# Kernel optimization log

Measured on AMD Instinct MI355X. Metric: run time of the kernel, lower is better.

Reference implementation:

```python
import jax, jax.numpy as jnp
import numpy as np
import math

H = 8
D_MODEL = 512
D_K = D_MODEL // H          # 64, per-head value dim
D_QK = D_K // 2             # 32, per-head query/key dim
B, S = 2, 4096


def setup_inputs() -> dict:
    key = jax.random.key(0)
    ks = jax.random.split(key, 20)
    std = 0.02
    inp = {
        'query': jax.random.normal(ks[0], (B, S, D_MODEL), jnp.float32),
        'key':   jax.random.normal(ks[1], (B, S, D_MODEL), jnp.float32),
        'value': jax.random.normal(ks[2], (B, S, D_MODEL), jnp.float32),
        # MLP_q: d_model -> 2*d_model -> d_model/2
        'Wq1': jax.random.normal(ks[3], (D_MODEL, 2 * D_MODEL), jnp.float32) * std,
        'bq1': jnp.zeros((2 * D_MODEL,), jnp.float32),
        'Wq2': jax.random.normal(ks[4], (2 * D_MODEL, D_MODEL // 2), jnp.float32) * std,
        'bq2': jnp.zeros((D_MODEL // 2,), jnp.float32),
        # MLP_k: d_model -> 2*d_model -> d_model/2
        'Wk1': jax.random.normal(ks[5], (D_MODEL, 2 * D_MODEL), jnp.float32) * std,
        'bk1': jnp.zeros((2 * D_MODEL,), jnp.float32),
        'Wk2': jax.random.normal(ks[6], (2 * D_MODEL, D_MODEL // 2), jnp.float32) * std,
        'bk2': jnp.zeros((D_MODEL // 2,), jnp.float32),
        # linear_v and output linear: d_model -> d_model
        'Wv': jax.random.normal(ks[7], (D_MODEL, D_MODEL), jnp.float32) * std,
        'bv': jnp.zeros((D_MODEL,), jnp.float32),
        'Wo': jax.random.normal(ks[8], (D_MODEL, D_MODEL), jnp.float32) * std,
        'bo': jnp.zeros((D_MODEL,), jnp.float32),
    }
    return inp


def reference(query, key, value, Wq1, bq1, Wq2, bq2, Wk1, bk1, Wk2, bk2, Wv, bv, Wo, bo):
    nb = query.shape[0]
    # MLP_q / MLP_k: Linear -> exact GELU -> Linear (torch GELU default is erf)
    q = jax.nn.gelu(query @ Wq1 + bq1, approximate=False) @ Wq2 + bq2   # [B,S,D_MODEL/2]
    k = jax.nn.gelu(key   @ Wk1 + bk1, approximate=False) @ Wk2 + bk2   # [B,S,D_MODEL/2]
    v = value @ Wv + bv                                                  # [B,S,D_MODEL]

    q = q.reshape(nb, -1, H, D_QK)   # [B,S,H,d_qk]
    k = k.reshape(nb, -1, H, D_QK)
    v = v.reshape(nb, -1, H, D_K)    # [B,S,H,d_k]

    # scores scaled by sqrt(d_qk) since query.size(-1) == d_k//2 in the original
    scores = jnp.einsum('bqhd,bkhd->bhqk', q, k) / math.sqrt(D_QK)  # [B,H,S,S]
    p = jax.nn.softmax(scores, axis=-1)
    x = jnp.einsum('bhqk,bkhd->bqhd', p, v).reshape(nb, -1, H * D_K)  # [B,S,D_MODEL]
    return x @ Wo + bo
```

## Files before the change

kernel.cpp:

```cpp
#include <hip/hip_runtime.h>
#include <math.h>

typedef __attribute__((ext_vector_type(8))) short short8;
typedef __bf16 bf16x8 __attribute__((ext_vector_type(8)));
typedef __attribute__((ext_vector_type(4))) float f32x4;
typedef __attribute__((ext_vector_type(2))) float f32x2;
typedef __attribute__((ext_vector_type(16))) float f32x16;
typedef __attribute__((ext_vector_type(4))) unsigned uint4v;

__device__ inline short f2bf(float f) {
    unsigned u = __builtin_bit_cast(unsigned, f);
    u += 0x7fff + ((u >> 16) & 1);
    return (short)(u >> 16);
}
__device__ inline float gelu_f(float x) {
    return 0.5f * x * (1.f + erff(x * 0.70710678118654752f));
}

__device__ inline void gload_lds16(const void* g, void* l) {
    __builtin_amdgcn_global_load_lds(
        (const __attribute__((address_space(1))) unsigned int*)g,
        (__attribute__((address_space(3))) unsigned int*)l, 16, 0, 0);
}

__global__ __launch_bounds__(256) void prep_w(
    const float* __restrict__ Wq1, const float* __restrict__ Wk1,
    const float* __restrict__ Wq2, const float* __restrict__ Wk2,
    const float* __restrict__ Wv,  const float* __restrict__ Wo,
    short* __restrict__ Wq1t, short* __restrict__ Wk1t,
    short* __restrict__ Wq2t, short* __restrict__ Wk2t,
    short* __restrict__ Wvt,  short* __restrict__ Wot)
{
    int id = blockIdx.x;
    const float* W; short* Wt; int K, N;
    if (id < 512)       { W = Wq1; Wt = Wq1t; K = 512;  N = 1024; }
    else if (id < 1024) { W = Wk1; Wt = Wk1t; K = 512;  N = 1024; id -= 512; }
    else if (id < 1280) { W = Wq2; Wt = Wq2t; K = 1024; N = 256;  id -= 1024; }
    else if (id < 1536) { W = Wk2; Wt = Wk2t; K = 1024; N = 256;  id -= 1280; }
    else if (id < 1792) { W = Wv;  Wt = Wvt;  K = 512;  N = 512;  id -= 1536; }
    else                { W = Wo;  Wt = Wot;  K = 512;  N = 512;  id -= 1792; }
    int nx = N >> 5;
    int n0 = (id % nx) * 32, k0 = (id / nx) * 32;

    __shared__ float T[32][33];
    int tid = threadIdx.x;
    int r = tid >> 3, c4 = (tid & 7) * 4;
    float4 v4 = *(const float4*)&W[(size_t)(k0 + r) * N + n0 + c4];
    T[r][c4 + 0] = v4.x; T[r][c4 + 1] = v4.y; T[r][c4 + 2] = v4.z; T[r][c4 + 3] = v4.w;
    __syncthreads();
    short4 o;
    o.x = f2bf(T[c4 + 0][r]);
    o.y = f2bf(T[c4 + 1][r]);
    o.z = f2bf(T[c4 + 2][r]);
    o.w = f2bf(T[c4 + 3][r]);
    *(short4*)&Wt[(size_t)(n0 + r) * K + k0 + c4] = o;
}

template <int BM, int BN, int AF32>
__device__ __forceinline__ void gemm_core(
    const void* __restrict__ A, const short* __restrict__ B,
    const float* __restrict__ bias, void* __restrict__ C_,
    float scale, int act, int om, int nbn, int N, int K, int L)
{
    constexpr int MT = BM / 32;
    constexpr int NT = BN / 32;
    const int xcd = L & 7;
    const int per = L >> 3;
    const int bn = (per % nbn) * BN;
    const int bm = ((per / nbn) * 8 + xcd) * BM;

    const int tid = threadIdx.x;
    const int w = tid >> 6;
    const int lane = tid & 63;
    const int l15 = lane & 15, quad = lane >> 4;
    const int wm = (w >> 1) * (BM / 2), wn = (w & 1) * (BN / 2);

    __shared__ __align__(16) short As[2][BM * 64];
    __shared__ __align__(16) short Bs[2][BN * 64];

    const float* Af = (const float*)A;
    const short* Ab = (const short*)A;

    float4 xa[BM / 32], ya[BM / 32];

    auto stage_issue = [&](int k0, int buf) {
#pragma unroll
        for (int i = 0; i < BM / 32; ++i) {
            int ga = tid + i * 256;
            int row = ga >> 3, g = ga & 7;
            if constexpr (AF32) {
                const float* src = &Af[(size_t)(bm + row) * K + k0 + ((g ^ (row & 7)) * 8)];
                xa[i] = *(const float4*)src;
                ya[i] = *(const float4*)(src + 4);
            } else {
                gload_lds16(&Ab[(size_t)(bm + row) * K + k0 + ((g ^ (row & 7)) * 8)],
                            &As[buf][(i * 256 + w * 64) * 8]);
            }
        }
#pragma unroll
        for (int i = 0; i < BN / 32; ++i) {
            int gb = tid + i * 256;
            int row = gb >> 3, g = gb & 7;
            gload_lds16(&B[(size_t)(bn + row) * K + k0 + ((g ^ (row & 7)) * 8)],
                        &Bs[buf][(i * 256 + w * 64) * 8]);
        }
    };
    auto stage_finish = [&](int buf) {
        asm volatile("s_waitcnt vmcnt(0)");
        if constexpr (AF32) {
#pragma unroll
            for (int i = 0; i < BM / 32; ++i) {
                int ga = tid + i * 256;
                int row = ga >> 3, g = ga & 7;
                unsigned u0, u1, u2, u3;
                asm("v_cvt_pk_bf16_f32 %0, %1, %2" : "=v"(u0) : "v"(xa[i].x), "v"(xa[i].y));
                asm("v_cvt_pk_bf16_f32 %0, %1, %2" : "=v"(u1) : "v"(xa[i].z), "v"(xa[i].w));
                asm("v_cvt_pk_bf16_f32 %0, %1, %2" : "=v"(u2) : "v"(ya[i].x), "v"(ya[i].y));
                asm("v_cvt_pk_bf16_f32 %0, %1, %2" : "=v"(u3) : "v"(ya[i].z), "v"(ya[i].w));
                uint4v u; u[0] = u0; u[1] = u1; u[2] = u2; u[3] = u3;
                *(uint4v*)(void*)&As[buf][row * 64 + g * 8] = u;
            }
        }
    };

    f32x4 acc[MT][NT];
#pragma unroll
    for (int mt = 0; mt < MT; ++mt)
#pragma unroll
        for (int nt = 0; nt < NT; ++nt) acc[mt][nt] = (f32x4){0.f, 0.f, 0.f, 0.f};

    const int ntile = K >> 6;

    stage_issue(0, 0);
    stage_finish(0);
    __syncthreads();

    int cur = 0;
    for (int t = 0; t < ntile; ++t) {
        const bool has_next = (t + 1 < ntile);
        if (has_next) stage_issue((t + 1) << 6, cur ^ 1);

        const short* Asc = As[cur];
        const short* Bsc = Bs[cur];
#pragma unroll
        for (int ks = 0; ks < 2; ++ks) {
            bf16x8 af[MT], bfr[NT];
#pragma unroll
            for (int t2 = 0; t2 < MT; ++t2) {
                int row = wm + t2 * 16 + l15;
                af[t2] = __builtin_bit_cast(bf16x8,
                    *(const short8*)(const void*)&Asc[row * 64 + (((ks * 4 + quad) ^ (row & 7)) * 8)]);
            }
#pragma unroll
            for (int t2 = 0; t2 < NT; ++t2) {
                int row = wn + t2 * 16 + l15;
                bfr[t2] = __builtin_bit_cast(bf16x8,
                    *(const short8*)(const void*)&Bsc[row * 64 + (((ks * 4 + quad) ^ (row & 7)) * 8)]);
            }
#pragma unroll
            for (int mt = 0; mt < MT; ++mt)
#pragma unroll
                for (int nt = 0; nt < NT; ++nt)
                    acc[mt][nt] = __builtin_amdgcn_mfma_f32_16x16x32_bf16(af[mt], bfr[nt], acc[mt][nt], 0, 0, 0);
        }

        if (has_next) stage_finish(cur ^ 1);
        __syncthreads();
        cur ^= 1;
    }

    float bvv[NT];
#pragma unroll
    for (int nt = 0; nt < NT; ++nt) bvv[nt] = bias[bn + wn + nt * 16 + l15];
#pragma unroll
    for (int mt = 0; mt < MT; ++mt)
#pragma unroll
        for (int r = 0; r < 4; ++r) {
            int row = bm + wm + mt * 16 + quad * 4 + r;
#pragma unroll
            for (int nt = 0; nt < NT; ++nt) {
                float v = acc[mt][nt][r] + bvv[nt];
                if (act) v = gelu_f(v);
                v *= scale;
                int col = bn + wn + nt * 16 + l15;
                if (om == 1) {
                    ((float*)C_)[(size_t)row * N + col] = v;
                } else if (om == 2) {
                    int b_ = row >> 12, key = row & 4095;
                    int kt = key >> 6, nt_ = (key >> 5) & 1, l31_ = key & 31;
                    int h_ = col >> 5, kcol = col & 31;
                    int ks_ = kcol >> 4, hi_ = (kcol >> 3) & 1, j_ = kcol & 7;
                    size_t idx = ((((size_t)(b_ * 8 + h_) * 64 + kt) * 4 +
                                   (nt_ * 2 + ks_)) * 64 + (hi_ * 32 + l31_)) * 8 + j_;
                    ((short*)C_)[idx] = f2bf(v);
                } else if (om == 3) {
                    int b_ = row >> 12, key = row & 4095;
                    int kt = key >> 6, keyr = key & 63;
                    int ks_ = keyr >> 4, hi_ = (keyr >> 3) & 1, j_ = keyr & 7;
                    int h_ = col >> 6, dk = col & 63;
                    int dt_ = dk >> 5, l31_ = dk & 31;
                    size_t idx = ((((size_t)(b_ * 8 + h_) * 64 + kt) * 8 +
                                   (dt_ * 4 + ks_)) * 64 + (hi_ * 32 + l31_)) * 8 + j_;
                    ((short*)C_)[idx] = f2bf(v);
                } else {
                    ((short*)C_)[(size_t)row * N + col] = f2bf(v);
                }
            }
        }
}

__global__ __launch_bounds__(256) void mega1(
    const float* __restrict__ q, const float* __restrict__ k,
    const float* __restrict__ v,
    const short* __restrict__ Wq1t, const short* __restrict__ Wk1t,
    const short* __restrict__ Wvt,
    const float* __restrict__ bq1, const float* __restrict__ bk1,
    const float* __restrict__ bv,
    short* __restrict__ H1q, short* __restrict__ H1k, short* __restrict__ vfr)
{
    const int z = blockIdx.z;
    if (z == 2 && blockIdx.x >= 256) return;
    const float* A   = z == 2 ? v    : (z == 1 ? k    : q);
    const short* B   = z == 2 ? Wvt  : (z == 1 ? Wk1t : Wq1t);
    const float* bia = z == 2 ? bv   : (z == 1 ? bk1  : bq1);
    void*        C   = z == 2 ? (void*)vfr : (z == 1 ? (void*)H1k : (void*)H1q);
    const int act = z == 2 ? 0 : 1;
    const int om  = z == 2 ? 3 : 0;
    const int nbn = z == 2 ? 4 : 8;
    const int N   = z == 2 ? 512 : 1024;
    gemm_core<128, 128, 1>(A, B, bia, C, 1.f, act, om, nbn, N, 512, blockIdx.x);
}

__global__ __launch_bounds__(256) void gemm2k(
    const short* __restrict__ H1q, const short* __restrict__ H1k,
    const short* __restrict__ Wq2t, const short* __restrict__ Wk2t,
    const float* __restrict__ bq2, const float* __restrict__ bk2,
    short* __restrict__ qbb, short* __restrict__ kfr, float qscale)
{
    const int z = blockIdx.z;
    const short* A   = z ? H1k : H1q;
    const short* B   = z ? Wk2t : Wq2t;
    const float* bia = z ? bk2 : bq2;
    void*        C   = z ? (void*)kfr : (void*)qbb;
    const float  sc  = z ? 1.f : qscale;
    const int    om  = z ? 2 : 0;
    gemm_core<64, 64, 0>(A, B, bia, C, sc, 0, om, 4, 256, 1024, blockIdx.x);
}

__global__ __launch_bounds__(256) void gemmok(
    const short* __restrict__ xbb, const short* __restrict__ Wot,
    const float* __restrict__ bo, float* __restrict__ out)
{
    gemm_core<64, 64, 0>(xbb, Wot, bo, out, 1.f, 0, 1, 8, 512, 512, blockIdx.x);
}

__global__ __launch_bounds__(256, 4) void flash_ks(
    const short* __restrict__ qb, const short* __restrict__ kfr,
    const short* __restrict__ vfr, short* __restrict__ xbb)
{
    const int L = blockIdx.x;
    const int xcd = L & 7;
    const int idx = L >> 3;
    const int bh = xcd * 2 + (idx & 1);
    const int qt = idx >> 1;
    const int b = bh >> 3, h = bh & 7;
    const int w = threadIdx.x >> 6;
    const int qg = w >> 1;
    const int kh = w & 1;
    const int lane = threadIdx.x & 63;
    const int l31 = lane & 31;
    const int half = lane >> 5;

    __shared__ __align__(16) char smem[17408];

    const short* qrow = qb + (size_t)(b * 4096 + qt * 64 + qg * 32 + l31) * 256 + h * 32 + half * 8;
    bf16x8 qf0 = __builtin_bit_cast(bf16x8, *(const short8*)(const void*)qrow);
    bf16x8 qf1 = __builtin_bit_cast(bf16x8, *(const short8*)(const void*)(qrow + 16));

    f32x16 O0{}, O1{};
    f32x2 lp = (f32x2){0.f, 0.f};

    const short* kbase = kfr + ((size_t)bh * 64) * 4 * 512 + lane * 8;
    const short* vbase = vfr + ((size_t)bh * 64) * 8 * 512 + lane * 8;

#pragma unroll 1
    for (int t = 0; t < 32; ++t) {
        const int kt = kh * 32 + t;
        bf16x8 kc[4], vc[8];
        const short* kp = kbase + (size_t)kt * 4 * 512;
        const short* vp = vbase + (size_t)kt * 8 * 512;
#pragma unroll
        for (int c = 0; c < 4; ++c)
            kc[c] = __builtin_bit_cast(bf16x8, *(const short8*)(const void*)(kp + c * 512));
#pragma unroll
        for (int c = 0; c < 8; ++c)
            vc[c] = __builtin_bit_cast(bf16x8, *(const short8*)(const void*)(vp + c * 512));

        f32x16 zero{};
        f32x16 s0 = __builtin_amdgcn_mfma_f32_32x32x16_bf16(kc[0], qf0, zero, 0, 0, 0);
        s0 = __builtin_amdgcn_mfma_f32_32x32x16_bf16(kc[1], qf1, s0, 0, 0, 0);
        f32x16 s1 = __builtin_amdgcn_mfma_f32_32x32x16_bf16(kc[2], qf0, zero, 0, 0, 0);
        s1 = __builtin_amdgcn_mfma_f32_32x32x16_bf16(kc[3], qf1, s1, 0, 0, 0);

        bf16x8 pf[4];
#pragma unroll
        for (int nt = 0; nt < 2; ++nt) {
            const f32x16& s = nt ? s1 : s0;
            float p0  = __builtin_amdgcn_exp2f(s[0]);
            float p1  = __builtin_amdgcn_exp2f(s[1]);
            float p2  = __builtin_amdgcn_exp2f(s[2]);
            float p3  = __builtin_amdgcn_exp2f(s[3]);
            float p4  = __builtin_amdgcn_exp2f(s[4]);
            float p5  = __builtin_amdgcn_exp2f(s[5]);
            float p6  = __builtin_amdgcn_exp2f(s[6]);
            float p7  = __builtin_amdgcn_exp2f(s[7]);
            float p8  = __builtin_amdgcn_exp2f(s[8]);
            float p9  = __builtin_amdgcn_exp2f(s[9]);
            float p10 = __builtin_amdgcn_exp2f(s[10]);
            float p11 = __builtin_amdgcn_exp2f(s[11]);
            float p12 = __builtin_amdgcn_exp2f(s[12]);
            float p13 = __builtin_amdgcn_exp2f(s[13]);
            float p14 = __builtin_amdgcn_exp2f(s[14]);
            float p15 = __builtin_amdgcn_exp2f(s[15]);

            lp += (f32x2){p0,  p1};
            lp += (f32x2){p2,  p3};
            lp += (f32x2){p4,  p5};
            lp += (f32x2){p6,  p7};
            lp += (f32x2){p8,  p9};
            lp += (f32x2){p10, p11};
            lp += (f32x2){p12, p13};
            lp += (f32x2){p14, p15};

            unsigned D0, D1, D2, D3, D4, D5, D6, D7;
            asm("v_cvt_pk_bf16_f32 %0, %1, %2" : "=v"(D0) : "v"(p0),  "v"(p1));
            asm("v_cvt_pk_bf16_f32 %0, %1, %2" : "=v"(D1) : "v"(p2),  "v"(p3));
            asm("v_cvt_pk_bf16_f32 %0, %1, %2" : "=v"(D2) : "v"(p4),  "v"(p5));
            asm("v_cvt_pk_bf16_f32 %0, %1, %2" : "=v"(D3) : "v"(p6),  "v"(p7));
            asm("v_cvt_pk_bf16_f32 %0, %1, %2" : "=v"(D4) : "v"(p8),  "v"(p9));
            asm("v_cvt_pk_bf16_f32 %0, %1, %2" : "=v"(D5) : "v"(p10), "v"(p11));
            asm("v_cvt_pk_bf16_f32 %0, %1, %2" : "=v"(D6) : "v"(p12), "v"(p13));
            asm("v_cvt_pk_bf16_f32 %0, %1, %2" : "=v"(D7) : "v"(p14), "v"(p15));
            asm("v_permlane32_swap_b32 %0, %1" : "+v"(D0), "+v"(D2));
            asm("v_permlane32_swap_b32 %0, %1" : "+v"(D1), "+v"(D3));
            asm("v_permlane32_swap_b32 %0, %1" : "+v"(D4), "+v"(D6));
            asm("v_permlane32_swap_b32 %0, %1" : "+v"(D5), "+v"(D7));
            uint4v u0; u0[0] = D0; u0[1] = D1; u0[2] = D2; u0[3] = D3;
            uint4v u1; u1[0] = D4; u1[1] = D5; u1[2] = D6; u1[3] = D7;
            pf[2 * nt + 0] = __builtin_bit_cast(bf16x8, u0);
            pf[2 * nt + 1] = __builtin_bit_cast(bf16x8, u1);
        }

#pragma unroll
        for (int ks = 0; ks < 4; ++ks) {
            O0 = __builtin_amdgcn_mfma_f32_32x32x16_bf16(pf[ks], vc[ks], O0, 0, 0, 0);
            O1 = __builtin_amdgcn_mfma_f32_32x32x16_bf16(pf[ks], vc[4 + ks], O1, 0, 0, 0);
        }
    }

    float lsum = lp[0] + lp[1];
    float lother = lsum;
    asm("v_permlane32_swap_b32 %0, %1" : "+v"(lsum), "+v"(lother));
    lsum += lother;

    float* redO = (float*)smem;
    float* redl = (float*)(smem + 16896);
    if (half == 0)
        redl[(qg * 2 + kh) * 32 + l31] = lsum;
    if (kh == 1) {
        float* Bo = redO + qg * 32 * 66;
#pragma unroll
        for (int r = 0; r < 16; ++r) {
            int q = (r & 3) + 8 * (r >> 2) + 4 * half;
            Bo[q * 66 + l31] = O0[r];
            Bo[q * 66 + 32 + l31] = O1[r];
        }
    }
    __syncthreads();
    if (kh == 0) {
        const float* Bo = redO + qg * 32 * 66;
#pragma unroll
        for (int r = 0; r < 16; ++r) {
            int q = (r & 3) + 8 * (r >> 2) + 4 * half;
            float o0 = O0[r] + Bo[q * 66 + l31];
            float o1 = O1[r] + Bo[q * 66 + 32 + l31];
            float inv = 1.f / (redl[(qg * 2 + 0) * 32 + q] + redl[(qg * 2 + 1) * 32 + q]);
            size_t row = (size_t)(b * 4096 + qt * 64 + qg * 32 + q);
            short* d = xbb + row * 512 + h * 64 + l31;
            d[0] = f2bf(o0 * inv);
            d[32] = f2bf(o1 * inv);
        }
    }
}

extern "C" void kernel_launch(void* const* d_in, const int* in_sizes, int n_in,
                              void* d_out, int out_size, void* d_ws, size_t ws_size,
                              hipStream_t stream)
{
    const float* query = (const float*)d_in[0];
    const float* key   = (const float*)d_in[1];
    const float* value = (const float*)d_in[2];
    const float* Wq1   = (const float*)d_in[3];
    const float* bq1   = (const float*)d_in[4];
    const float* Wq2   = (const float*)d_in[5];
    const float* bq2   = (const float*)d_in[6];
    const float* Wk1   = (const float*)d_in[7];
    const float* bk1   = (const float*)d_in[8];
    const float* Wk2   = (const float*)d_in[9];
    const float* bk2   = (const float*)d_in[10];
    const float* Wv    = (const float*)d_in[11];
    const float* bv    = (const float*)d_in[12];
    const float* Wo    = (const float*)d_in[13];
    const float* bo    = (const float*)d_in[14];
    float* out = (float*)d_out;

    char* ws = (char*)d_ws;
    short* H1q   = (short*)(ws + 0);
    short* H1k   = (short*)(ws + 16777216);
    short* xbb   = (short*)(ws + 0);
    short* qbb   = (short*)(ws + 33554432);
    short* kfr   = (short*)(ws + 50331648);
    short* vfr   = (short*)(ws + 54525952);
    short* Wq1t  = (short*)(ws + 62914560);
    short* Wk1t  = (short*)(ws + 63963136);
    short* Wq2t  = (short*)(ws + 65011712);
    short* Wk2t  = (short*)(ws + 65536000);
    short* Wvt   = (short*)(ws + 66060288);
    short* Wot   = (short*)(ws + 66584576);

    dim3 blk(256);
    const float qscale = 0.17677669529663687f * 1.4426950408889634f;

    prep_w<<<dim3(2048), blk, 0, stream>>>(
        Wq1, Wk1, Wq2, Wk2, Wv, Wo, Wq1t, Wk1t, Wq2t, Wk2t, Wvt, Wot);

    mega1<<<dim3(512, 1, 3), blk, 0, stream>>>(
        query, key, value, Wq1t, Wk1t, Wvt, bq1, bk1, bv, H1q, H1k, vfr);

    gemm2k<<<dim3(512, 1, 2), blk, 0, stream>>>(
        H1q, H1k, Wq2t, Wk2t, bq2, bk2, qbb, kfr, qscale);

    flash_ks<<<dim3(1024), blk, 0, stream>>>(qbb, kfr, vfr, xbb);

    gemmok<<<dim3(1024), blk, 0, stream>>>(xbb, Wot, bo, out);
}
```

Before: 302.1 us.

## Unroll GEMM double-buffer loop by two and shrink mega1 tiles to 64x64

The GEMM main loop is restructured into an explicit two-stage ping-pong over separate LDS buffers. The blanket vmcnt(0) wait is dropped from the finish step, so waiting now relies on the compiler. The first-layer projection kernel switches from 128x128 to 64x64 tiles with four times as many blocks, aiming for better occupancy and load balance. Smaller tiles reduce data reuse and raise global traffic. Removing the explicit wait also risks LDS races for async global-to-LDS loads, and the unrolled loop assumes an even tile count.

```diff
diff --git a/kernel.cpp b/kernel.cpp
--- a/kernel.cpp
+++ b/kernel.cpp
@@ -75,15 +75,15 @@
     const int l15 = lane & 15, quad = lane >> 4;
     const int wm = (w >> 1) * (BM / 2), wn = (w & 1) * (BN / 2);
 
-    __shared__ __align__(16) short As[2][BM * 64];
-    __shared__ __align__(16) short Bs[2][BN * 64];
+    __shared__ __align__(16) short As0[BM * 64], As1[BM * 64];
+    __shared__ __align__(16) short Bs0[BN * 64], Bs1[BN * 64];
 
     const float* Af = (const float*)A;
     const short* Ab = (const short*)A;
 
     float4 xa[BM / 32], ya[BM / 32];
 
-    auto stage_issue = [&](int k0, int buf) {
+    auto issue = [&](int k0, short* Asb, short* Bsb) {
 #pragma unroll
         for (int i = 0; i < BM / 32; ++i) {
             int ga = tid + i * 256;
@@ -94,7 +94,7 @@
                 ya[i] = *(const float4*)(src + 4);
             } else {
                 gload_lds16(&Ab[(size_t)(bm + row) * K + k0 + ((g ^ (row & 7)) * 8)],
-                            &As[buf][(i * 256 + w * 64) * 8]);
+                            &Asb[(i * 256 + w * 64) * 8]);
             }
         }
 #pragma unroll
@@ -102,11 +102,10 @@
             int gb = tid + i * 256;
             int row = gb >> 3, g = gb & 7;
             gload_lds16(&B[(size_t)(bn + row) * K + k0 + ((g ^ (row & 7)) * 8)],
-                        &Bs[buf][(i * 256 + w * 64) * 8]);
+                        &Bsb[(i * 256 + w * 64) * 8]);
         }
     };
-    auto stage_finish = [&](int buf) {
-        asm volatile("s_waitcnt vmcnt(0)");
+    auto finishA = [&](short* Asb) {
         if constexpr (AF32) {
 #pragma unroll
             for (int i = 0; i < BM / 32; ++i) {
@@ -118,7 +117,7 @@
                 asm("v_cvt_pk_bf16_f32 %0, %1, %2" : "=v"(u2) : "v"(ya[i].x), "v"(ya[i].y));
                 asm("v_cvt_pk_bf16_f32 %0, %1, %2" : "=v"(u3) : "v"(ya[i].z), "v"(ya[i].w));
                 uint4v u; u[0] = u0; u[1] = u1; u[2] = u2; u[3] = u3;
-                *(uint4v*)(void*)&As[buf][row * 64 + g * 8] = u;
+                *(uint4v*)(void*)&Asb[row * 64 + g * 8] = u;
             }
         }
     };
@@ -129,19 +128,7 @@
 #pragma unroll
         for (int nt = 0; nt < NT; ++nt) acc[mt][nt] = (f32x4){0.f, 0.f, 0.f, 0.f};
 
-    const int ntile = K >> 6;
-
-    stage_issue(0, 0);
-    stage_finish(0);
-    __syncthreads();
-
-    int cur = 0;
-    for (int t = 0; t < ntile; ++t) {
-        const bool has_next = (t + 1 < ntile);
-        if (has_next) stage_issue((t + 1) << 6, cur ^ 1);
-
-        const short* Asc = As[cur];
-        const short* Bsc = Bs[cur];
+    auto compute = [&](const short* Asc, const short* Bsc) {
 #pragma unroll
         for (int ks = 0; ks < 2; ++ks) {
             bf16x8 af[MT], bfr[NT];
@@ -163,10 +150,23 @@
                 for (int nt = 0; nt < NT; ++nt)
                     acc[mt][nt] = __builtin_amdgcn_mfma_f32_16x16x32_bf16(af[mt], bfr[nt], acc[mt][nt], 0, 0, 0);
         }
-
-        if (has_next) stage_finish(cur ^ 1);
+    };
+
+    const int ntile = K >> 6;
+
+    issue(0, As0, Bs0);
+    finishA(As0);
+    __syncthreads();
+
+    for (int t = 0; t < ntile; t += 2) {
+        issue((t + 1) << 6, As1, Bs1);
+        compute(As0, Bs0);
+        finishA(As1);
         __syncthreads();
-        cur ^= 1;
+        if (t + 2 < ntile) issue((t + 2) << 6, As0, Bs0);
+        compute(As1, Bs1);
+        if (t + 2 < ntile) finishA(As0);
+        __syncthreads();
     }
 
     float bvv[NT];
@@ -219,16 +219,16 @@
     short* __restrict__ H1q, short* __restrict__ H1k, short* __restrict__ vfr)
 {
     const int z = blockIdx.z;
-    if (z == 2 && blockIdx.x >= 256) return;
+    if (z == 2 && blockIdx.x >= 1024) return;
     const float* A   = z == 2 ? v    : (z == 1 ? k    : q);
     const short* B   = z == 2 ? Wvt  : (z == 1 ? Wk1t : Wq1t);
     const float* bia = z == 2 ? bv   : (z == 1 ? bk1  : bq1);
     void*        C   = z == 2 ? (void*)vfr : (z == 1 ? (void*)H1k : (void*)H1q);
     const int act = z == 2 ? 0 : 1;
     const int om  = z == 2 ? 3 : 0;
-    const int nbn = z == 2 ? 4 : 8;
+    const int nbn = z == 2 ? 8 : 16;
     const int N   = z == 2 ? 512 : 1024;
-    gemm_core<128, 128, 1>(A, B, bia, C, 1.f, act, om, nbn, N, 512, blockIdx.x);
+    gemm_core<64, 64, 1>(A, B, bia, C, 1.f, act, om, nbn, N, 512, blockIdx.x);
 }
 
 __global__ __launch_bounds__(256) void gemm2k(
@@ -434,7 +434,7 @@
     prep_w<<<dim3(2048), blk, 0, stream>>>(
         Wq1, Wk1, Wq2, Wk2, Wv, Wo, Wq1t, Wk1t, Wq2t, Wk2t, Wvt, Wot);
 
-    mega1<<<dim3(512, 1, 3), blk, 0, stream>>>(
+    mega1<<<dim3(2048, 1, 3), blk, 0, stream>>>(
         query, key, value, Wq1t, Wk1t, Wvt, bq1, bk1, bv, H1q, H1k, vfr);
 
     gemm2k<<<dim3(512, 1, 2), blk, 0, stream>>>(
```

Result: faster. 257.6 us (-14.7%).
